# Kernel tuning notes

Hardware: AMD Instinct MI355X
Metric: run time of the kernel (lower is better)

## Reference

```python
import jax, jax.numpy as jnp
import numpy as np

H, D_MODEL, D_K, D_V = 16, 1024, 64, 64
B, S = 4, 2048


def _xavier(key, shape):
    # xavier_uniform over last two dims (matches torch for 3D param: fan per matrix)
    fan_in, fan_out = shape[-2], shape[-1]
    limit = jnp.sqrt(6.0 / (fan_in + fan_out))
    return jax.random.uniform(key, shape, jnp.float32, -limit, limit)


def setup_inputs() -> dict:
    key = jax.random.key(0)
    kq, kk, kv, kwq, kwk, kwv, kwo = jax.random.split(key, 7)
    return {
        "Q": jax.random.normal(kq, (B, S, D_MODEL), jnp.float32),
        "K": jax.random.normal(kk, (B, S, D_MODEL), jnp.float32),
        "V": jax.random.normal(kv, (B, S, D_MODEL), jnp.float32),
        "W_Q": _xavier(kwq, (H, D_MODEL, D_K)),
        "W_K": _xavier(kwk, (H, D_MODEL, D_K)),
        "W_V": _xavier(kwv, (H, D_MODEL, D_V)),
        "W_O": _xavier(kwo, (H * D_V, D_MODEL)),
    }


def reference(Q, K, V, W_Q, W_K, W_V, W_O):
    # Per-head projections (batched over heads instead of Python loop)
    q = jnp.einsum("bsm,hmk->bhsk", Q, W_Q)  # [B,H,S,d_k]
    k = jnp.einsum("bsm,hmk->bhsk", K, W_K)  # [B,H,S,d_k]
    v = jnp.einsum("bsm,hmv->bhsv", V, W_V)  # [B,H,S,d_v]

    scale = 1.0 / jnp.sqrt(jnp.asarray(q.shape[-1], q.dtype))
    scores = jnp.einsum("bhqk,bhsk->bhqs", q, k) * scale  # [B,H,S,S]
    attn = jax.nn.softmax(scores, axis=-1)
    heads = jnp.einsum("bhqs,bhsv->bhqv", attn, v)  # [B,H,S,d_v]

    # concat heads along feature dim: [B,S,H*d_v]
    concat = jnp.transpose(heads, (0, 2, 1, 3)).reshape(Q.shape[0], Q.shape[1], -1)
    return concat @ W_O  # [B,S,d_model]
```

## Files before the change

kernel.cpp:

```cpp
#include <hip/hip_runtime.h>
#include <hip/hip_bf16.h>


typedef __attribute__((ext_vector_type(8))) short short8;
typedef __attribute__((ext_vector_type(4))) float floatx4;
typedef unsigned short u16;

#define NH 16
#define DM 1024
#define DK 64
#define NB 4
#define SS 2048

__device__ inline u16 f2bf(float f) {
    unsigned u = __builtin_bit_cast(unsigned, f);
    return (u16)((u + 0x7fffu + ((u >> 16) & 1u)) >> 16);
}

__device__ inline unsigned pk2(float a, float b) {
    unsigned r;
    asm("v_cvt_pk_bf16_f32 %0, %1, %2" : "=v"(r) : "v"(a), "v"(b));
    return r;
}

__device__ inline uint4 cvt8r(float4 lo, float4 hi) {
    uint4 r;
    r.x = pk2(lo.x, lo.y);
    r.y = pk2(lo.z, lo.w);
    r.z = pk2(hi.x, hi.y);
    r.w = pk2(hi.z, hi.w);
    return r;
}

__device__ inline void lds_barrier() {
    asm volatile("s_waitcnt lgkmcnt(0)" ::: "memory");
    __builtin_amdgcn_s_barrier();
    __builtin_amdgcn_sched_barrier(0);
}

__global__ __launch_bounds__(256) void prep_w(
    const float* __restrict__ W0, const float* __restrict__ W1,
    const float* __restrict__ W2, const float* __restrict__ WO,
    uint4* __restrict__ dst, int mode) {
    int idx = blockIdx.x * 256 + threadIdx.x;
    const int total = mode ? 128 * 1024 : 3 * 16 * 128 * 64;
    const int stride = gridDim.x * 256;
    for (; idx < total; idx += stride) {
        float v[8];
        if (mode == 0) {
            int n64 = idx & 63, kt = (idx >> 6) & 127;
            int h = (idx >> 13) & 15, w = idx >> 17;
            const float* src = (w == 0 ? W0 : (w == 1 ? W1 : W2)) +
                               ((size_t)(h * 1024 + kt * 8)) * 64 + n64;
#pragma unroll
            for (int j = 0; j < 8; j++) v[j] = src[(size_t)j * 64];
        } else {
            int n = idx & 1023, kt = idx >> 10;
            const float* src = WO + (size_t)(kt * 8) * 1024 + n;
#pragma unroll
            for (int j = 0; j < 8; j++) v[j] = src[(size_t)j * 1024];
        }
        uint4 r;
        r.x = pk2(v[0], v[1]);
        r.y = pk2(v[2], v[3]);
        r.z = pk2(v[4], v[5]);
        r.w = pk2(v[6], v[7]);
        dst[idx] = r;
    }
}

__global__ __launch_bounds__(256, 4) void proj_pre(
    const float* __restrict__ X0, const float* __restrict__ X1,
    const float* __restrict__ X2, const uint4* __restrict__ wb,
    u16* __restrict__ outb) {
    __shared__ u16 a_s[2][64][40];
    const int bid = blockIdx.x;
    const int work = (bid & 7) * 384 + (bid >> 3);
    const int z = work >> 10;
    const int rem = work & 1023;
    const int mtile = rem >> 3;
    const int ntile = rem & 7;
    const float* X = z == 0 ? X0 : (z == 1 ? X1 : X2);
    u16* out = outb + (size_t)z * ((size_t)NB * NH * SS * DK);
    const int t = threadIdx.x;
    const int w = t >> 6, lane = t & 63, quad = lane >> 4, lr = lane & 15;
    const int ar = t >> 2, ac = (t & 3) * 8;
    const int h = ntile * 2 + (w >> 1);
    const int nh = (w & 1) * 32;
    const size_t bbase = (((size_t)z * 16 + h) * 128 + quad) * 64 + nh + lr;

    float4 axl, axh;
    {
        const float* ap = &X[(size_t)(mtile * 64 + ar) * DM + ac];
        axl = *(const float4*)ap;
        axh = *(const float4*)(ap + 4);
    }
    uint4 bcur[2], bnx[2];
    bcur[0] = wb[bbase];
    bcur[1] = wb[bbase + 16];
    floatx4 acc[4][2] = {};
    int cur = 0;
    for (int kki = 0; kki < DM / 32; kki++) {
        *(uint4*)&a_s[cur][ar][ac] = cvt8r(axl, axh);
        if (kki + 1 < DM / 32) {
            const float* ap =
                &X[(size_t)(mtile * 64 + ar) * DM + (kki + 1) * 32 + ac];
            axl = *(const float4*)ap;
            axh = *(const float4*)(ap + 4);
            const size_t bi = bbase + (size_t)(kki + 1) * 256;
            bnx[0] = wb[bi];
            bnx[1] = wb[bi + 16];
        }
        lds_barrier();
        short8 af[4];
#pragma unroll
        for (int i = 0; i < 4; i++)
            af[i] = *(const short8*)&a_s[cur][i * 16 + lr][quad * 8];
#pragma unroll
        for (int i = 0; i < 4; i++)
#pragma unroll
            for (int j = 0; j < 2; j++)
                acc[i][j] = __builtin_amdgcn_mfma_f32_16x16x32_bf16(
                    af[i], __builtin_bit_cast(short8, bcur[j]), acc[i][j],
                    0, 0, 0);
        bcur[0] = bnx[0];
        bcur[1] = bnx[1];
        cur ^= 1;
    }

    const int b = (mtile * 64) >> 11;
#pragma unroll
    for (int i = 0; i < 4; i++)
#pragma unroll
        for (int j = 0; j < 2; j++)
#pragma unroll
            for (int rg = 0; rg < 4; rg++) {
                int m = mtile * 64 + i * 16 + quad * 4 + rg;
                int s = m & (SS - 1);
                out[((size_t)(b * NH + h) * SS + s) * DK + nh + j * 16 + lr] =
                    f2bf(acc[i][j][rg]);
            }
}

__global__ __launch_bounds__(256, 4) void oproj_pre(
    const u16* __restrict__ heads,
    const uint4* __restrict__ wob,
    float* __restrict__ out) {
    __shared__ u16 a_s[2][64][40];
    const int bid = blockIdx.x;
    const int work = (bid & 7) * 128 + (bid >> 3);
    const int mtile = work >> 3;
    const int ntile = work & 7;
    const int t = threadIdx.x;
    const int w = t >> 6, lane = t & 63, quad = lane >> 4, lr = lane & 15;
    const int ar = t >> 2, ac = (t & 3) * 8;
    const int b = (mtile * 64) >> 11;
    const int nb = ntile * 128 + w * 32;
    const size_t bbase = (size_t)quad * 1024 + nb + lr;

    uint4 areg;
    {
        int m = mtile * 64 + ar, s = m & (SS - 1);
        areg = *(const uint4*)&heads[((size_t)(b * NH + 0) * SS + s) * DK + ac];
    }
    uint4 bcur[2], bnx[2];
    bcur[0] = wob[bbase];
    bcur[1] = wob[bbase + 16];
    floatx4 acc[4][2] = {};
    int cur = 0;
    for (int kki = 0; kki < DM / 32; kki++) {
        *(uint4*)&a_s[cur][ar][ac] = areg;
        if (kki + 1 < DM / 32) {
            const int kk = (kki + 1) * 32;
            const int hh = kk >> 6, dvb = kk & 63;
            int m = mtile * 64 + ar, s = m & (SS - 1);
            areg = *(const uint4*)&heads[((size_t)(b * NH + hh) * SS + s) * DK +
                                         dvb + ac];
            const size_t bi = bbase + (size_t)(kki + 1) * 4 * 1024;
            bnx[0] = wob[bi];
            bnx[1] = wob[bi + 16];
        }
        lds_barrier();
        short8 af[4];
#pragma unroll
        for (int i = 0; i < 4; i++)
            af[i] = *(const short8*)&a_s[cur][i * 16 + lr][quad * 8];
#pragma unroll
        for (int i = 0; i < 4; i++)
#pragma unroll
            for (int j = 0; j < 2; j++)
                acc[i][j] = __builtin_amdgcn_mfma_f32_16x16x32_bf16(
                    af[i], __builtin_bit_cast(short8, bcur[j]), acc[i][j],
                    0, 0, 0);
        bcur[0] = bnx[0];
        bcur[1] = bnx[1];
        cur ^= 1;
    }

#pragma unroll
    for (int i = 0; i < 4; i++)
#pragma unroll
        for (int j = 0; j < 2; j++)
#pragma unroll
            for (int rg = 0; rg < 4; rg++) {
                int m = mtile * 64 + i * 16 + quad * 4 + rg;
                out[(size_t)m * DM + nb + j * 16 + lr] = acc[i][j][rg];
            }
}

__global__ __launch_bounds__(256, 2) void proj_gemm(
    const float* __restrict__ X,
    const float* __restrict__ W,
    u16* __restrict__ out) {
    __shared__ u16 a_s[128][38];
    __shared__ u16 b_s[128][38];
    const int mtile = blockIdx.x, ntile = blockIdx.y;
    const int t = threadIdx.x;
    const int w = t >> 6, lane = t & 63, quad = lane >> 4, lr = lane & 15;
    const int wm = w & 1, wn = w >> 1;
    const int ar = t >> 2, ac = (t & 3) * 8;
    const int bk = t >> 3, bn = (t & 7) * 8;

    float4 axl[2], axh[2], bwl[2], bwh[2];
#define PROJ_PREF(kk)                                                          \
    {                                                                          \
        _Pragma("unroll") for (int it = 0; it < 2; it++) {                     \
            const float* ap =                                                  \
                &X[(size_t)(mtile * 128 + ar + 64 * it) * DM + (kk) + ac];     \
            axl[it] = *(const float4*)ap;                                      \
            axh[it] = *(const float4*)(ap + 4);                                \
            const float* bp =                                                  \
                &W[((size_t)(ntile * 2 + it) * DM + (kk) + bk) * DK + bn];     \
            bwl[it] = *(const float4*)bp;                                      \
            bwh[it] = *(const float4*)(bp + 4);                                \
        }                                                                      \
    }

    PROJ_PREF(0);
    floatx4 acc[4][4] = {};
    for (int kki = 0; kki < DM / 32; kki++) {
#pragma unroll
        for (int it = 0; it < 2; it++) {
            *(uint4*)&a_s[ar + 64 * it][ac] = cvt8r(axl[it], axh[it]);
            uint4 wv = cvt8r(bwl[it], bwh[it]);
            alignas(16) u16 tmp[8];
            *(uint4*)tmp = wv;
#pragma unroll
            for (int j = 0; j < 8; j++) b_s[64 * it + bn + j][bk] = tmp[j];
        }
        __syncthreads();
        if (kki + 1 < DM / 32) PROJ_PREF((kki + 1) * 32);
        short8 af[4], bf[4];
#pragma unroll
        for (int i = 0; i < 4; i++)
            af[i] = *(const short8*)&a_s[wm * 64 + i * 16 + lr][quad * 8];
#pragma unroll
        for (int j = 0; j < 4; j++)
            bf[j] = *(const short8*)&b_s[wn * 64 + j * 16 + lr][quad * 8];
#pragma unroll
        for (int i = 0; i < 4; i++)
#pragma unroll
            for (int j = 0; j < 4; j++)
                acc[i][j] = __builtin_amdgcn_mfma_f32_16x16x32_bf16(
                    af[i], bf[j], acc[i][j], 0, 0, 0);
        __syncthreads();
    }
#undef PROJ_PREF

    const int b = (mtile * 128) >> 11;
    const int h = ntile * 2 + wn;
#pragma unroll
    for (int i = 0; i < 4; i++)
#pragma unroll
        for (int j = 0; j < 4; j++)
#pragma unroll
            for (int rg = 0; rg < 4; rg++) {
                int m = mtile * 128 + wm * 64 + i * 16 + quad * 4 + rg;
                int s = m & (SS - 1);
                out[((size_t)(b * NH + h) * SS + s) * DK + j * 16 + lr] =
                    f2bf(acc[i][j][rg]);
            }
}

__global__ __launch_bounds__(256) void transpose_v(
    const u16* __restrict__ src, u16* __restrict__ dst) {
    __shared__ u16 ts[64][70];
    const int bh = blockIdx.x, st = blockIdx.y;
    const int t = threadIdx.x;
    const int r = t >> 3, c0 = (t & 7) * 8;
#pragma unroll
    for (int it = 0; it < 2; it++)
        *(uint4*)&ts[r + 32 * it][c0] =
            *(const uint4*)&src[((size_t)bh * SS + st * 64 + r + 32 * it) * DK + c0];
    __syncthreads();
#pragma unroll
    for (int it = 0; it < 2; it++) {
        int dv = r + 32 * it;
        alignas(16) u16 tmp[8];
#pragma unroll
        for (int j = 0; j < 8; j++) tmp[j] = ts[c0 + j][dv];
        *(uint4*)&dst[((size_t)bh * DK + dv) * SS + st * 64 + c0] = *(uint4*)tmp;
    }
}

#define SWZ(r, c) (((r) << 6) + ((c) ^ (((r) & 7) << 3)))

template <bool VT>
__global__ __launch_bounds__(256, 4) void attn_k(
    const u16* q, const u16* __restrict__ k,
    const u16* __restrict__ v, u16* o) {
    __shared__ u16 k_s[64 * 64];
    __shared__ u16 vt_s[64 * 64];

    const int bh = blockIdx.x, qt = blockIdx.y;
    const int t = threadIdx.x;
    const int w = t >> 6, lane = t & 63, quad = lane >> 4, lr = lane & 15;
    const size_t base = (size_t)bh * SS * DK;
    const size_t tbase = (size_t)bh * DK * SS;

    short8 aq[2][2];
#pragma unroll
    for (int qg = 0; qg < 2; qg++) {
        const size_t qrow =
            base + (size_t)(qt * 128 + w * 32 + qg * 16 + lr) * DK;
        aq[qg][0] = *(const short8*)&q[qrow + quad * 8];
        aq[qg][1] = *(const short8*)&q[qrow + 32 + quad * 8];
    }

    floatx4 o_acc[2][4] = {};
    float l0 = 0.f, l1 = 0.f;
    const int sr = t >> 3, sd = (t & 7) * 8;

    const float C1 = 0.18033688f;

    for (int kt = 0; kt < SS / 64; kt++) {
#pragma unroll
        for (int it = 0; it < 2; it++) {
            int r = sr + 32 * it;
            *(uint4*)&k_s[SWZ(r, sd)] =
                *(const uint4*)&k[base + (size_t)(kt * 64 + r) * DK + sd];
            if (VT) {
                *(uint4*)&vt_s[SWZ(r, sd)] =
                    *(const uint4*)&v[tbase + (size_t)r * SS + kt * 64 + sd];
            } else {
                uint4 vv = *(const uint4*)&v[base + (size_t)(kt * 64 + r) * DK + sd];
                alignas(16) u16 tmp[8];
                *(uint4*)tmp = vv;
#pragma unroll
                for (int j = 0; j < 8; j++) vt_s[SWZ(sd + j, r)] = tmp[j];
            }
        }
        __syncthreads();

        floatx4 s0[4] = {}, s1[4] = {};
#pragma unroll
        for (int ks = 0; ks < 2; ks++)
#pragma unroll
            for (int nt = 0; nt < 4; nt++) {
                short8 af =
                    *(const short8*)&k_s[SWZ(nt * 16 + lr, ks * 32 + quad * 8)];
                s0[nt] = __builtin_amdgcn_mfma_f32_16x16x32_bf16(
                    af, aq[0][ks], s0[nt], 0, 0, 0);
                s1[nt] = __builtin_amdgcn_mfma_f32_16x16x32_bf16(
                    af, aq[1][ks], s1[nt], 0, 0, 0);
            }

        unsigned W0[4][2], W1[4][2];
#pragma unroll
        for (int nt = 0; nt < 4; nt++) {
            float p0 = __builtin_amdgcn_exp2f(s0[nt][0] * C1);
            float p1 = __builtin_amdgcn_exp2f(s0[nt][1] * C1);
            float p2 = __builtin_amdgcn_exp2f(s0[nt][2] * C1);
            float p3 = __builtin_amdgcn_exp2f(s0[nt][3] * C1);
            l0 += (p0 + p1) + (p2 + p3);
            W0[nt][0] = pk2(p0, p1);
            W0[nt][1] = pk2(p2, p3);
            float q0 = __builtin_amdgcn_exp2f(s1[nt][0] * C1);
            float q1 = __builtin_amdgcn_exp2f(s1[nt][1] * C1);
            float q2 = __builtin_amdgcn_exp2f(s1[nt][2] * C1);
            float q3 = __builtin_amdgcn_exp2f(s1[nt][3] * C1);
            l1 += (q0 + q1) + (q2 + q3);
            W1[nt][0] = pk2(q0, q1);
            W1[nt][1] = pk2(q2, q3);
        }

        uint4 bf0[2], bf1[2];
#pragma unroll
        for (int ks = 0; ks < 2; ks++) {
            unsigned a0 = W0[2 * ks][0], b0 = W0[2 * ks + 1][0];
            unsigned a1 = W0[2 * ks][1], b1 = W0[2 * ks + 1][1];
            asm("v_permlane32_swap_b32 %0, %1" : "+v"(a0), "+v"(b0));
            asm("v_permlane16_swap_b32 %0, %1" : "+v"(a0), "+v"(b0));
            asm("v_permlane32_swap_b32 %0, %1" : "+v"(a1), "+v"(b1));
            asm("v_permlane16_swap_b32 %0, %1" : "+v"(a1), "+v"(b1));
            bf0[ks].x = a0; bf0[ks].y = a1; bf0[ks].z = b0; bf0[ks].w = b1;
            unsigned c0 = W1[2 * ks][0], d0 = W1[2 * ks + 1][0];
            unsigned c1 = W1[2 * ks][1], d1 = W1[2 * ks + 1][1];
            asm("v_permlane32_swap_b32 %0, %1" : "+v"(c0), "+v"(d0));
            asm("v_permlane16_swap_b32 %0, %1" : "+v"(c0), "+v"(d0));
            asm("v_permlane32_swap_b32 %0, %1" : "+v"(c1), "+v"(d1));
            asm("v_permlane16_swap_b32 %0, %1" : "+v"(c1), "+v"(d1));
            bf1[ks].x = c0; bf1[ks].y = c1; bf1[ks].z = d0; bf1[ks].w = d1;
        }

#pragma unroll
        for (int ks = 0; ks < 2; ks++) {
            short8 p0f = __builtin_bit_cast(short8, bf0[ks]);
            short8 p1f = __builtin_bit_cast(short8, bf1[ks]);
#pragma unroll
            for (int nt = 0; nt < 4; nt++) {
                short8 afv =
                    *(const short8*)&vt_s[SWZ(nt * 16 + lr, ks * 32 + quad * 8)];
                o_acc[0][nt] = __builtin_amdgcn_mfma_f32_16x16x32_bf16(
                    afv, p0f, o_acc[0][nt], 0, 0, 0);
                o_acc[1][nt] = __builtin_amdgcn_mfma_f32_16x16x32_bf16(
                    afv, p1f, o_acc[1][nt], 0, 0, 0);
            }
        }
        __syncthreads();
    }

    l0 += __shfl_xor(l0, 16);
    l0 += __shfl_xor(l0, 32);
    l1 += __shfl_xor(l1, 16);
    l1 += __shfl_xor(l1, 32);
    float inv0 = 1.0f / l0, inv1 = 1.0f / l1;

    const size_t orow0 = base + (size_t)(qt * 128 + w * 32 + lr) * DK;
    const size_t orow1 = orow0 + (size_t)16 * DK;
#pragma unroll
    for (int nt = 0; nt < 4; nt++) {
        uint2 pk;
        pk.x = pk2(o_acc[0][nt][0] * inv0, o_acc[0][nt][1] * inv0);
        pk.y = pk2(o_acc[0][nt][2] * inv0, o_acc[0][nt][3] * inv0);
        *(uint2*)&o[orow0 + nt * 16 + quad * 4] = pk;
        pk.x = pk2(o_acc[1][nt][0] * inv1, o_acc[1][nt][1] * inv1);
        pk.y = pk2(o_acc[1][nt][2] * inv1, o_acc[1][nt][3] * inv1);
        *(uint2*)&o[orow1 + nt * 16 + quad * 4] = pk;
    }
}

__global__ __launch_bounds__(256, 2) void oproj(
    const u16* __restrict__ heads,
    const float* __restrict__ WO,
    float* __restrict__ out) {
    __shared__ u16 a_s[128][38];
    __shared__ u16 b_s[128][38];
    const int mtile = blockIdx.x, ntile = blockIdx.y;
    const int t = threadIdx.x;
    const int w = t >> 6, lane = t & 63, quad = lane >> 4, lr = lane & 15;
    const int wm = w & 1, wn = w >> 1;
    const int ar = t >> 2, ac = (t & 3) * 8;
    const int bk = t >> 3, bn = (t & 7) * 8;
    const int b = (mtile * 128) >> 11;

    uint4 areg[2];
    float4 bwl[2], bwh[2];
#define OP_PREF(kk)                                                            \
    {                                                                          \
        const int h = (kk) >> 6, dvb = (kk) & 63;                              \
        _Pragma("unroll") for (int it = 0; it < 2; it++) {                     \
            int m = mtile * 128 + ar + 64 * it, s = m & (SS - 1);              \
            areg[it] = *(const uint4*)                                         \
                &heads[((size_t)(b * NH + h) * SS + s) * DK + dvb + ac];       \
            const float* bp =                                                  \
                &WO[(size_t)((kk) + bk) * DM + ntile * 128 + 64 * it + bn];    \
            bwl[it] = *(const float4*)bp;                                      \
            bwh[it] = *(const float4*)(bp + 4);                                \
        }                                                                      \
    }

    OP_PREF(0);
    floatx4 acc[4][4] = {};
    for (int kki = 0; kki < DM / 32; kki++) {
#pragma unroll
        for (int it = 0; it < 2; it++) {
            *(uint4*)&a_s[ar + 64 * it][ac] = areg[it];
            uint4 wv = cvt8r(bwl[it], bwh[it]);
            alignas(16) u16 tmp[8];
            *(uint4*)tmp = wv;
#pragma unroll
            for (int j = 0; j < 8; j++) b_s[64 * it + bn + j][bk] = tmp[j];
        }
        __syncthreads();
        if (kki + 1 < DM / 32) OP_PREF((kki + 1) * 32);
        short8 af[4], bf[4];
#pragma unroll
        for (int i = 0; i < 4; i++)
            af[i] = *(const short8*)&a_s[wm * 64 + i * 16 + lr][quad * 8];
#pragma unroll
        for (int j = 0; j < 4; j++)
            bf[j] = *(const short8*)&b_s[wn * 64 + j * 16 + lr][quad * 8];
#pragma unroll
        for (int i = 0; i < 4; i++)
#pragma unroll
            for (int j = 0; j < 4; j++)
                acc[i][j] = __builtin_amdgcn_mfma_f32_16x16x32_bf16(
                    af[i], bf[j], acc[i][j], 0, 0, 0);
        __syncthreads();
    }
#undef OP_PREF

#pragma unroll
    for (int i = 0; i < 4; i++)
#pragma unroll
        for (int j = 0; j < 4; j++)
#pragma unroll
            for (int rg = 0; rg < 4; rg++) {
                int m = mtile * 128 + wm * 64 + i * 16 + quad * 4 + rg;
                int n = ntile * 128 + wn * 64 + j * 16 + lr;
                out[(size_t)m * DM + n] = acc[i][j][rg];
            }
}

extern "C" void kernel_launch(void* const* d_in, const int* in_sizes, int n_in,
                              void* d_out, int out_size, void* d_ws, size_t ws_size,
                              hipStream_t stream) {
    const float* Q  = (const float*)d_in[0];
    const float* K  = (const float*)d_in[1];
    const float* V  = (const float*)d_in[2];
    const float* WQ = (const float*)d_in[3];
    const float* WK = (const float*)d_in[4];
    const float* WV = (const float*)d_in[5];
    const float* WO = (const float*)d_in[6];
    float* out = (float*)d_out;

    char* ws = (char*)d_ws;
    const size_t NQKV = (size_t)NB * NH * SS * DK;
    const size_t SZ = NQKV * 2;
    u16* qp  = (u16*)ws;
    u16* kp  = (u16*)(ws + SZ);
    u16* vp  = (u16*)(ws + 2 * SZ);
    u16* vtp = (u16*)(ws + 3 * SZ);
    u16* hp  = qp;

    const size_t WB_SZ  = 3ull * 16 * 128 * 64 * sizeof(uint4);
    const size_t WOB_SZ = 128ull * 1024 * sizeof(uint4);
    const bool tierA = ws_size >= 4 * SZ + WB_SZ + WOB_SZ;
    const bool tierB = !tierA && ws_size >= 4 * SZ;

    if (tierA || tierB) {
        uint4* wb  = tierA ? (uint4*)(ws + 4 * SZ) : (uint4*)vtp;
        uint4* wob = tierA ? (uint4*)(ws + 4 * SZ + WB_SZ) : (uint4*)kp;

        prep_w<<<1536, 256, 0, stream>>>(WQ, WK, WV, WO, wb, 0);
        if (tierA) prep_w<<<512, 256, 0, stream>>>(WQ, WK, WV, WO, wob, 1);

        proj_pre<<<dim3(3072), 256, 0, stream>>>(Q, K, V, wb, qp);
        transpose_v<<<dim3(NB * NH, SS / 64), 256, 0, stream>>>(vp, vtp);
        attn_k<true><<<dim3(NB * NH, SS / 128), 256, 0, stream>>>(
            qp, kp, vtp, hp);
        if (tierB) prep_w<<<512, 256, 0, stream>>>(WQ, WK, WV, WO, wob, 1);
        oproj_pre<<<dim3(1024), 256, 0, stream>>>(hp, wob, out);
    } else {
        dim3 pg(NB * SS / 128, DM / 128);
        proj_gemm<<<pg, 256, 0, stream>>>(Q, WQ, qp);
        proj_gemm<<<pg, 256, 0, stream>>>(K, WK, kp);
        proj_gemm<<<pg, 256, 0, stream>>>(V, WV, vp);
        attn_k<false><<<dim3(NB * NH, SS / 128), 256, 0, stream>>>(
            qp, kp, vp, hp);
        oproj<<<dim3(NB * SS / 128, DM / 128), 256, 0, stream>>>(hp, WO, out);
    }
}
```

Before: 347.1 us.

## Load GEMM A-fragments directly from global memory, dropping LDS staging and barriers

The projection and output-projection GEMM kernels no longer stage A tiles through shared memory with a barrier each k-step. Each lane now loads its MFMA A fragment straight from global memory, which means each wave redundantly loads the full 64-row A tile. Loads are double-buffered in registers with a two-stage software pipeline. This removes the LDS round-trip and the block-level synchronisation, at the cost of four times more global/L2 traffic for A and more registers, with occupancy lowered from 4 to 3 blocks in proj_pre.

```diff
diff --git a/kernel.cpp b/kernel.cpp
--- a/kernel.cpp
+++ b/kernel.cpp
@@ -30,12 +30,6 @@
     r.z = pk2(hi.x, hi.y);
     r.w = pk2(hi.z, hi.w);
     return r;
-}
-
-__device__ inline void lds_barrier() {
-    asm volatile("s_waitcnt lgkmcnt(0)" ::: "memory");
-    __builtin_amdgcn_s_barrier();
-    __builtin_amdgcn_sched_barrier(0);
 }
 
 __global__ __launch_bounds__(256) void prep_w(
@@ -69,11 +63,10 @@
     }
 }
 
-__global__ __launch_bounds__(256, 4) void proj_pre(
+__global__ __launch_bounds__(256, 3) void proj_pre(
     const float* __restrict__ X0, const float* __restrict__ X1,
     const float* __restrict__ X2, const uint4* __restrict__ wb,
     u16* __restrict__ outb) {
-    __shared__ u16 a_s[2][64][40];
     const int bid = blockIdx.x;
     const int work = (bid & 7) * 384 + (bid >> 3);
     const int z = work >> 10;
@@ -84,49 +77,50 @@
     u16* out = outb + (size_t)z * ((size_t)NB * NH * SS * DK);
     const int t = threadIdx.x;
     const int w = t >> 6, lane = t & 63, quad = lane >> 4, lr = lane & 15;
-    const int ar = t >> 2, ac = (t & 3) * 8;
     const int h = ntile * 2 + (w >> 1);
     const int nh = (w & 1) * 32;
     const size_t bbase = (((size_t)z * 16 + h) * 128 + quad) * 64 + nh + lr;
 
-    float4 axl, axh;
-    {
-        const float* ap = &X[(size_t)(mtile * 64 + ar) * DM + ac];
-        axl = *(const float4*)ap;
-        axh = *(const float4*)(ap + 4);
-    }
-    uint4 bcur[2], bnx[2];
-    bcur[0] = wb[bbase];
-    bcur[1] = wb[bbase + 16];
+    const float* arow[4];
+#pragma unroll
+    for (int i = 0; i < 4; i++)
+        arow[i] = &X[(size_t)(mtile * 64 + i * 16 + lr) * DM + quad * 8];
+
+    float4 al0[4], ah0[4], al1[4], ah1[4];
+    uint4 b0[2], b1[2];
     floatx4 acc[4][2] = {};
-    int cur = 0;
-    for (int kki = 0; kki < DM / 32; kki++) {
-        *(uint4*)&a_s[cur][ar][ac] = cvt8r(axl, axh);
-        if (kki + 1 < DM / 32) {
-            const float* ap =
-                &X[(size_t)(mtile * 64 + ar) * DM + (kki + 1) * 32 + ac];
-            axl = *(const float4*)ap;
-            axh = *(const float4*)(ap + 4);
-            const size_t bi = bbase + (size_t)(kki + 1) * 256;
-            bnx[0] = wb[bi];
-            bnx[1] = wb[bi + 16];
-        }
-        lds_barrier();
-        short8 af[4];
-#pragma unroll
-        for (int i = 0; i < 4; i++)
-            af[i] = *(const short8*)&a_s[cur][i * 16 + lr][quad * 8];
-#pragma unroll
-        for (int i = 0; i < 4; i++)
-#pragma unroll
-            for (int j = 0; j < 2; j++)
-                acc[i][j] = __builtin_amdgcn_mfma_f32_16x16x32_bf16(
-                    af[i], __builtin_bit_cast(short8, bcur[j]), acc[i][j],
-                    0, 0, 0);
-        bcur[0] = bnx[0];
-        bcur[1] = bnx[1];
-        cur ^= 1;
-    }
+
+#define PPRF(AL, AH, BB, kk)                                                   \
+    {                                                                          \
+        _Pragma("unroll") for (int i = 0; i < 4; i++) {                        \
+            AL[i] = *(const float4*)(arow[i] + (size_t)(kk) * 32);             \
+            AH[i] = *(const float4*)(arow[i] + (size_t)(kk) * 32 + 4);         \
+        }                                                                      \
+        BB[0] = wb[bbase + (size_t)(kk) * 256];                                \
+        BB[1] = wb[bbase + (size_t)(kk) * 256 + 16];                           \
+    }
+#define PCMP(AL, AH, BB)                                                       \
+    {                                                                          \
+        short8 af[4];                                                          \
+        _Pragma("unroll") for (int i = 0; i < 4; i++)                          \
+            af[i] = __builtin_bit_cast(short8, cvt8r(AL[i], AH[i]));           \
+        _Pragma("unroll") for (int i = 0; i < 4; i++)                          \
+            _Pragma("unroll") for (int j = 0; j < 2; j++)                      \
+                acc[i][j] = __builtin_amdgcn_mfma_f32_16x16x32_bf16(           \
+                    af[i], __builtin_bit_cast(short8, BB[j]), acc[i][j],       \
+                    0, 0, 0);                                                  \
+    }
+
+    PPRF(al0, ah0, b0, 0);
+    PPRF(al1, ah1, b1, 1);
+    for (int kki = 0; kki < DM / 32; kki += 2) {
+        PCMP(al0, ah0, b0);
+        if (kki + 2 < DM / 32) PPRF(al0, ah0, b0, kki + 2);
+        PCMP(al1, ah1, b1);
+        if (kki + 3 < DM / 32) PPRF(al1, ah1, b1, kki + 3);
+    }
+#undef PPRF
+#undef PCMP
 
     const int b = (mtile * 64) >> 11;
 #pragma unroll
@@ -146,56 +140,54 @@
     const u16* __restrict__ heads,
     const uint4* __restrict__ wob,
     float* __restrict__ out) {
-    __shared__ u16 a_s[2][64][40];
     const int bid = blockIdx.x;
     const int work = (bid & 7) * 128 + (bid >> 3);
     const int mtile = work >> 3;
     const int ntile = work & 7;
     const int t = threadIdx.x;
     const int w = t >> 6, lane = t & 63, quad = lane >> 4, lr = lane & 15;
-    const int ar = t >> 2, ac = (t & 3) * 8;
     const int b = (mtile * 64) >> 11;
     const int nb = ntile * 128 + w * 32;
     const size_t bbase = (size_t)quad * 1024 + nb + lr;
 
-    uint4 areg;
-    {
-        int m = mtile * 64 + ar, s = m & (SS - 1);
-        areg = *(const uint4*)&heads[((size_t)(b * NH + 0) * SS + s) * DK + ac];
-    }
-    uint4 bcur[2], bnx[2];
-    bcur[0] = wob[bbase];
-    bcur[1] = wob[bbase + 16];
+    const u16* arow[4];
+#pragma unroll
+    for (int i = 0; i < 4; i++) {
+        int s = (mtile * 64 + i * 16 + lr) & (SS - 1);
+        arow[i] = &heads[((size_t)(b * NH) * SS + s) * DK + quad * 8];
+    }
+
+    uint4 a0[4], a1[4], b0[2], b1[2];
     floatx4 acc[4][2] = {};
-    int cur = 0;
-    for (int kki = 0; kki < DM / 32; kki++) {
-        *(uint4*)&a_s[cur][ar][ac] = areg;
-        if (kki + 1 < DM / 32) {
-            const int kk = (kki + 1) * 32;
-            const int hh = kk >> 6, dvb = kk & 63;
-            int m = mtile * 64 + ar, s = m & (SS - 1);
-            areg = *(const uint4*)&heads[((size_t)(b * NH + hh) * SS + s) * DK +
-                                         dvb + ac];
-            const size_t bi = bbase + (size_t)(kki + 1) * 4 * 1024;
-            bnx[0] = wob[bi];
-            bnx[1] = wob[bi + 16];
-        }
-        lds_barrier();
-        short8 af[4];
-#pragma unroll
-        for (int i = 0; i < 4; i++)
-            af[i] = *(const short8*)&a_s[cur][i * 16 + lr][quad * 8];
-#pragma unroll
-        for (int i = 0; i < 4; i++)
-#pragma unroll
-            for (int j = 0; j < 2; j++)
-                acc[i][j] = __builtin_amdgcn_mfma_f32_16x16x32_bf16(
-                    af[i], __builtin_bit_cast(short8, bcur[j]), acc[i][j],
-                    0, 0, 0);
-        bcur[0] = bnx[0];
-        bcur[1] = bnx[1];
-        cur ^= 1;
-    }
+
+#define OAOFF(kk) ((size_t)((kk) >> 1) * SS * DK + (size_t)((kk) & 1) * 32)
+#define OPRF(AA, BB, kk)                                                       \
+    {                                                                          \
+        _Pragma("unroll") for (int i = 0; i < 4; i++)                          \
+            AA[i] = *(const uint4*)(arow[i] + OAOFF(kk));                      \
+        BB[0] = wob[bbase + (size_t)(kk) * 4096];                              \
+        BB[1] = wob[bbase + (size_t)(kk) * 4096 + 16];                         \
+    }
+#define OCMP(AA, BB)                                                           \
+    {                                                                          \
+        _Pragma("unroll") for (int i = 0; i < 4; i++)                          \
+            _Pragma("unroll") for (int j = 0; j < 2; j++)                      \
+                acc[i][j] = __builtin_amdgcn_mfma_f32_16x16x32_bf16(           \
+                    __builtin_bit_cast(short8, AA[i]),                         \
+                    __builtin_bit_cast(short8, BB[j]), acc[i][j], 0, 0, 0);    \
+    }
+
+    OPRF(a0, b0, 0);
+    OPRF(a1, b1, 1);
+    for (int kki = 0; kki < DM / 32; kki += 2) {
+        OCMP(a0, b0);
+        if (kki + 2 < DM / 32) OPRF(a0, b0, kki + 2);
+        OCMP(a1, b1);
+        if (kki + 3 < DM / 32) OPRF(a1, b1, kki + 3);
+    }
+#undef OPRF
+#undef OCMP
+#undef OAOFF
 
 #pragma unroll
     for (int i = 0; i < 4; i++)
@@ -203,8 +195,8 @@
         for (int j = 0; j < 2; j++)
 #pragma unroll
             for (int rg = 0; rg < 4; rg++) {
-                int m = mtile * 64 + i * 16 + quad * 4 + rg;
-                out[(size_t)m * DM + nb + j * 16 + lr] = acc[i][j][rg];
+                int mm = mtile * 64 + i * 16 + quad * 4 + rg;
+                out[(size_t)mm * DM + nb + j * 16 + lr] = acc[i][j][rg];
             }
 }
 
```

Result: slower. 638.2 us (+83.9%).
